# Kernel optimization log

Hardware: AMD Instinct MI355X
Metric: run time of the kernel (lower is better)

## Reference

```python
import jax, jax.numpy as jnp
import numpy as np
from itertools import product

EPS = 1e-6
P = 3  # heatmap_size; corr channels = P**3 = 27


def l2_on_axis(x, axis=1):
    return jnp.sqrt(jnp.sum(x * x, axis=axis, keepdims=True) + EPS)


def reduce_masked_mean(x, mask):
    return jnp.sum(x * mask) / (jnp.sum(mask) + EPS)


def smoothl1(d):
    a = jnp.abs(d)
    return jnp.where(a < 1.0, 0.5 * d * d, a - 0.5)


def corr3d(f0, f1):
    # 3D correlation volume, patch P^3, zero padding. (B,C,D,H,W)->(B,P^3,D,H,W)
    B, C, D, H, W = f0.shape
    pad = P // 2
    f1p = jnp.pad(f1, ((0, 0), (0, 0), (pad, pad), (pad, pad), (pad, pad)))
    outs = []
    for dz in range(P):
        for dy in range(P):
            for dx in range(P):
                s = f1p[:, :, dz:dz + D, dy:dy + H, dx:dx + W]
                outs.append(jnp.einsum('bcdhw,bcdhw->bdhw', f0, s))
    return jnp.stack(outs, axis=1)


def flow_head(cc, W1, b1, W2, b2):
    cc = jax.nn.relu(cc)
    cc = cc / (jnp.sqrt(jnp.sum(cc * cc, axis=1, keepdims=True)) + EPS)  # l2_normalize dim=1
    h = jnp.einsum('oc,bcdhw->bodhw', W1, cc) + b1[None, :, None, None, None]
    h = jnp.where(h > 0, h, 0.01 * h)  # LeakyReLU
    return jnp.einsum('oc,bcdhw->bodhw', W2, h) + b2[None, :, None, None, None]


def backwarp(feat, flow):
    # trilinear backwarp, zero padding outside; flow ch: (dx->W, dy->H, dz->D)
    B, C, D, H, W = feat.shape
    zz, yy, xx = jnp.meshgrid(jnp.arange(D, dtype=flow.dtype),
                              jnp.arange(H, dtype=flow.dtype),
                              jnp.arange(W, dtype=flow.dtype), indexing='ij')
    xs = xx[None] + flow[:, 0]
    ys = yy[None] + flow[:, 1]
    zs = zz[None] + flow[:, 2]
    x0, y0, z0 = jnp.floor(xs), jnp.floor(ys), jnp.floor(zs)
    featf = feat.reshape(B, C, D * H * W)
    out = jnp.zeros_like(feat)
    for cz, cy, cx in product((0, 1), (0, 1), (0, 1)):
        zi, yi, xi = z0 + cz, y0 + cy, x0 + cx
        w = (1 - jnp.abs(zs - zi)) * (1 - jnp.abs(ys - yi)) * (1 - jnp.abs(xs - xi))
        valid = ((zi >= 0) & (zi < D) & (yi >= 0) & (yi < H) & (xi >= 0) & (xi < W)).astype(feat.dtype)
        idx = ((jnp.clip(zi, 0, D - 1) * H + jnp.clip(yi, 0, H - 1)) * W
               + jnp.clip(xi, 0, W - 1)).astype(jnp.int32).reshape(B, -1)
        g = jnp.take_along_axis(featf, idx[:, None, :], axis=2).reshape(B, C, D, H, W)
        out = out + g * (w * valid)[:, None]
    return out


def gradient3d_abs(x):
    dz = jnp.abs(jnp.pad(x[:, :, 1:] - x[:, :, :-1], ((0, 0), (0, 0), (0, 1), (0, 0), (0, 0))))
    dy = jnp.abs(jnp.pad(x[:, :, :, 1:] - x[:, :, :, :-1], ((0, 0), (0, 0), (0, 0), (0, 1), (0, 0))))
    dx = jnp.abs(jnp.pad(x[:, :, :, :, 1:] - x[:, :, :, :, :-1], ((0, 0), (0, 0), (0, 0), (0, 0), (0, 1))))
    return dx, dy, dz


def setup_inputs() -> dict:
    key = jax.random.key(0)
    ks = jax.random.split(key, 8)
    B, C, D, H, W = 2, 32, 64, 64, 64
    return {
        'feat0': jax.random.normal(ks[0], (B, C, D, H, W), jnp.float32),
        'feat1': jax.random.normal(ks[1], (B, C, D, H, W), jnp.float32),
        'flow_g': jax.random.normal(ks[2], (B, 3, D, H, W), jnp.float32),
        'mask_g': jax.random.uniform(ks[3], (B, 1, D, H, W), jnp.float32),
        'W1': jax.random.normal(ks[4], (64, P ** 3), jnp.float32) * 0.05,
        'b1': jnp.zeros((64,), jnp.float32),
        'W2': jax.random.normal(ks[5], (3, 64), jnp.float32) * 0.05,
        'b2': jnp.zeros((3,), jnp.float32),
        'is_synth': 0,
    }


def reference(feat0, feat1, flow_g, mask_g, W1, b1, W2, b2, is_synth):
    B, C, D, H, W = feat0.shape
    # hinge loss (feat1_aligned == feat1 at iteration 0)
    hinge_vox = jax.nn.relu(0.2 - l2_on_axis(feat1 - feat0))
    hinge_mask = (jnp.sum(jnp.abs(flow_g), axis=1, keepdims=True) > 1.0).astype(feat0.dtype)
    hinge_loss = reduce_masked_mean(hinge_vox, hinge_mask)

    # single scale sc=1.0
    flow_forw = flow_head(corr3d(feat0, feat1), W1, b1, W2, b2)
    flow_back = flow_head(corr3d(feat1, feat0), W1, b1, W2, b2)

    feat1_aligned = backwarp(feat1, flow_forw)
    ones1 = jnp.ones((B, 1, D, H, W), feat0.dtype)
    valid1 = backwarp(ones1, flow_forw)
    valid0 = backwarp(ones1, flow_forw)  # faithful: source also uses flow_total_forw

    feat_diff = reduce_masked_mean(l2_on_axis(feat1_aligned - feat0), valid1 * valid0)
    warp_loss_cumu = feat_diff  # * sc (=1)

    l1_diff = jnp.mean(smoothl1(flow_forw - flow_g), axis=1, keepdims=True)
    l2_diff = jnp.mean((flow_forw - flow_g) ** 2, axis=1, keepdims=True)
    nonzero = (jnp.sum(jnp.abs(flow_g), axis=1, keepdims=True) > 0.01).astype(feat0.dtype) * mask_g
    yeszero = (1.0 - nonzero) * mask_g
    l1_bal = 0.5 * (reduce_masked_mean(l1_diff, nonzero) + reduce_masked_mean(l1_diff, yeszero))
    l2_bal = 0.5 * (reduce_masked_mean(l2_diff, nonzero) + reduce_masked_mean(l2_diff, yeszero))

    fb_al = backwarp(flow_back, jax.lax.stop_gradient(flow_forw))
    ff_al = backwarp(flow_forw, jax.lax.stop_gradient(flow_back))
    cycle_loss = jnp.mean(smoothl1(flow_forw + fb_al)) + jnp.mean(smoothl1(flow_back + ff_al))

    dx, dy, dz = gradient3d_abs(flow_forw)
    smooth_forw = jnp.mean(dx + dy + dx, axis=1, keepdims=True)  # faithful: dx counted twice
    dx, dy, dz = gradient3d_abs(flow_back)
    smooth_back = jnp.mean(dx + dy + dx, axis=1, keepdims=True)
    smooth_loss = jnp.mean((smooth_forw + smooth_back) * 0.5)

    # all hyp coefficients = 1.0; is_synth selects identical coeffs here
    total_loss = hinge_loss + cycle_loss + l1_bal + l2_bal + warp_loss_cumu + smooth_loss
    return total_loss, flow_forw
```

## Files before the change

### kernel.cpp

```cpp
#include <hip/hip_runtime.h>
#include <math.h>

#define EPSF 1e-6f

typedef __attribute__((ext_vector_type(8))) short short8;
typedef __attribute__((ext_vector_type(4))) float f32x4;

constexpr int Bn = 2, Cn = 32, Dn = 64, Hn = 64, Wn = 64;
constexpr int HW  = Hn * Wn;
constexpr int DHW = Dn * HW;
constexpr int NVOX = Bn * DHW;
constexpr size_t BS = (size_t)Cn * DHW;


__device__ inline float sl1(float d) {
    float a = fabsf(d);
    return a < 1.f ? 0.5f * d * d : a - 0.5f;
}

__device__ inline int xcd_swz(int bid, int chunk) {
    return (bid & 7) * chunk + (bid >> 3);
}

__device__ inline float dpp_left(float v) {
    int r = __builtin_amdgcn_update_dpp(0, __float_as_int(v), 0x138, 0xF, 0xF, true);
    return __int_as_float(r);
}
__device__ inline float dpp_right(float v) {
    int r = __builtin_amdgcn_update_dpp(0, __float_as_int(v), 0x130, 0xF, 0xF, true);
    return __int_as_float(r);
}

__device__ inline unsigned int bf16b(float f) {
    return (__float_as_uint(f) + 0x8000u) >> 16;
}
__device__ inline unsigned int bfpack(float lo, float hi) {
    return bf16b(lo) | ((__float_as_uint(hi) + 0x8000u) & 0xffff0000u);
}
__device__ inline float bf2f(unsigned short u) {
    return __uint_as_float((unsigned int)u << 16);
}
__device__ inline float unpk(uint2 q, int j) {
    unsigned w = (j < 2) ? q.x : q.y;
    return (j & 1) ? __uint_as_float(w & 0xffff0000u)
                   : __uint_as_float(w << 16);
}

struct PairGather {
    int   pidx[4];
    int   sel[4];
    float w0[4], w1[4];
};

__device__ inline void warp_pair_setup(float flx, float fly, float flz,
                                       int x, int y, int z,
                                       PairGather& pg, float& wsum) {
    float xs = (float)x + flx, ys = (float)y + fly, zs = (float)z + flz;
    float xf = floorf(xs), yf = floorf(ys), zf = floorf(zs);
    float fx = xs - xf, fy = ys - yf, fz = zs - zf;
    int xi = (int)xf, yi = (int)yf, zi = (int)zf;

    int x0c = min(max(xi, 0), Wn - 1);
    bool xv0 = (xi >= 0) && (xi < Wn);
    bool xv1 = (xi + 1 >= 0) && (xi + 1 < Wn);
    int sel = (xi >= 0 && xi < Wn - 1) ? 1 : 0;
    float wx0 = xv0 ? (1.f - fx) : 0.f;
    float wx1 = xv1 ? fx : 0.f;

    wsum = 0.f;
#pragma unroll
    for (int cz = 0; cz < 2; cz++) {
        int zz = zi + cz;
        bool zv = (zz >= 0) && (zz < Dn);
        int zc = min(max(zz, 0), Dn - 1);
        float wz = (cz ? fz : 1.f - fz) * (zv ? 1.f : 0.f);
#pragma unroll
        for (int cy = 0; cy < 2; cy++) {
            int yy = yi + cy;
            bool yv = (yy >= 0) && (yy < Hn);
            int yc = min(max(yy, 0), Hn - 1);
            float wy = (cy ? fy : 1.f - fy) * (yv ? 1.f : 0.f);
            int k = cz * 2 + cy;
            int sp = (zc * Hn + yc) * Wn + x0c;
            pg.pidx[k] = min(sp, DHW - 2);
            pg.sel[k] = sel;
            float wzy = wz * wy;
            pg.w0[k] = wzy * wx0;
            pg.w1[k] = wzy * wx1;
            wsum += pg.w0[k] + pg.w1[k];
        }
    }
}

__device__ inline float gather8(const float* __restrict__ slab, const PairGather& pg) {
    float g = 0.f;
#pragma unroll
    for (int k = 0; k < 4; k++) {
        float2 v = *reinterpret_cast<const float2*>(slab + pg.pidx[k]);
        float second = pg.sel[k] ? v.y : v.x;
        g = fmaf(v.x, pg.w0[k], g);
        g = fmaf(second, pg.w1[k], g);
    }
    return g;
}

__global__ void prep_kernel(const float* __restrict__ W1, ushort* __restrict__ W1bf) {
    int i = blockIdx.x * 256 + threadIdx.x;
    if (i < 64 * 32) {
        int n = i >> 5, k = i & 31;
        float val = (k < 27) ? W1[n * 27 + k] : 0.f;
        W1bf[n * 40 + k] = (ushort)bf16b(val);
    }
}

__global__ __launch_bounds__(256)
void pack_kernel(const float* __restrict__ f1, uint2* __restrict__ pk1) {
    int v = blockIdx.x * 256 + threadIdx.x;
    int b = v >> 18;
    int sp = v & (DHW - 1);
    const float* src = f1 + (size_t)b * BS + sp;
#pragma unroll
    for (int p = 0; p < 8; p++) {
        float c0 = src[(size_t)(4 * p + 0) * DHW];
        float c1 = src[(size_t)(4 * p + 1) * DHW];
        float c2 = src[(size_t)(4 * p + 2) * DHW];
        float c3 = src[(size_t)(4 * p + 3) * DHW];
        pk1[(size_t)p * NVOX + v] = make_uint2(bfpack(c0, c1), bfpack(c2, c3));
    }
}

__device__ __forceinline__ void flow_head_mfma(
        float* acc, ushort (*ccS)[64][40], int wid, int lane,
        const ushort* __restrict__ W1bf, const float* __restrict__ b1,
        const float* __restrict__ W2, const float* __restrict__ b2,
        float* __restrict__ flow_out, size_t fb0,
        float& mfx, float& mfy, float& mfz) {
    float ss = 0.f;
#pragma unroll
    for (int i = 0; i < 27; i++) {
        float r = acc[i] > 0.f ? acc[i] : 0.f;
        acc[i] = r;
        ss = fmaf(r, r, ss);
    }
    float inv = 1.0f / (sqrtf(ss) + EPSF);
#pragma unroll
    for (int i = 0; i < 27; i++) acc[i] *= inv;

    {
        unsigned int pk[16];
#pragma unroll
        for (int i = 0; i < 13; i++) pk[i] = bfpack(acc[2 * i], acc[2 * i + 1]);
        pk[13] = bfpack(acc[26], 0.f);
        pk[14] = 0u; pk[15] = 0u;
        uint2* rowp = reinterpret_cast<uint2*>(&ccS[wid][lane][0]);
#pragma unroll
        for (int i = 0; i < 8; i++) rowp[i] = make_uint2(pk[2 * i], pk[2 * i + 1]);
    }

    int c0 = lane & 15, oct = lane >> 4;

    short8 bfr[4];
#pragma unroll
    for (int t = 0; t < 4; t++)
        bfr[t] = *reinterpret_cast<const short8*>(W1bf + (size_t)(t * 16 + c0) * 40 + oct * 8);

    f32x4 b1v[4], w2f0[4], w2f1[4], w2f2[4];
#pragma unroll
    for (int mt = 0; mt < 4; mt++) {
        b1v[mt]  = *reinterpret_cast<const f32x4*>(b1 + mt * 16 + oct * 4);
        w2f0[mt] = *reinterpret_cast<const f32x4*>(W2 + mt * 16 + oct * 4);
        w2f1[mt] = *reinterpret_cast<const f32x4*>(W2 + 64 + mt * 16 + oct * 4);
        w2f2[mt] = *reinterpret_cast<const f32x4*>(W2 + 128 + mt * 16 + oct * 4);
    }
    float bb0 = b2[0], bb1 = b2[1], bb2 = b2[2];

#pragma unroll
    for (int nt = 0; nt < 4; nt++) {
        short8 afr = *reinterpret_cast<const short8*>(&ccS[wid][nt * 16 + c0][oct * 8]);
        f32x4 ac[4];
#pragma unroll
        for (int mt = 0; mt < 4; mt++) {
            f32x4 zero = {0.f, 0.f, 0.f, 0.f};
            ac[mt] = __builtin_amdgcn_mfma_f32_16x16x32_bf16(bfr[mt], afr, zero, 0, 0, 0);
        }
        float p0 = 0.f, p1 = 0.f, p2 = 0.f;
#pragma unroll
        for (int mt = 0; mt < 4; mt++) {
#pragma unroll
            for (int rg = 0; rg < 4; rg++) {
                float h = ac[mt][rg] + b1v[mt][rg];
                h = fmaxf(h, 0.01f * h);
                p0 = fmaf(w2f0[mt][rg], h, p0);
                p1 = fmaf(w2f1[mt][rg], h, p1);
                p2 = fmaf(w2f2[mt][rg], h, p2);
            }
        }
        p0 += __shfl_xor(p0, 16); p0 += __shfl_xor(p0, 32);
        p1 += __shfl_xor(p1, 16); p1 += __shfl_xor(p1, 32);
        p2 += __shfl_xor(p2, 16); p2 += __shfl_xor(p2, 32);
        if (oct == nt) {
            int vox = nt * 16 + c0;
            mfx = p0 + bb0; mfy = p1 + bb1; mfz = p2 + bb2;
            flow_out[fb0 + vox]           = mfx;
            flow_out[fb0 + DHW + vox]     = mfy;
            flow_out[fb0 + 2 * DHW + vox] = mfz;
        }
    }
}

__device__ __forceinline__ void fwd_losses_common(
        float mfx, float mfy, float mfz, float diff2,
        const float* __restrict__ flow_g, const float* __restrict__ mask_g,
        int lane, int y, int z, int b, size_t fb0, float* pv) {
    size_t fbase = fb0 + lane;
    float gx = flow_g[fbase], gy = flow_g[fbase + DHW], gz = flow_g[fbase + 2 * DHW];
    float mg = mask_g[(size_t)b * DHW + (size_t)z * HW + y * Wn + lane];

    float ag = fabsf(gx) + fabsf(gy) + fabsf(gz);
    float hmask = ag > 1.0f ? 1.f : 0.f;
    float hv = 0.2f - sqrtf(diff2 + EPSF);
    hv = hv > 0.f ? hv : 0.f;

    float dx0 = mfx - gx, dy0 = mfy - gy, dz0 = mfz - gz;
    float l1 = (sl1(dx0) + sl1(dy0) + sl1(dz0)) * (1.f / 3.f);
    float l2 = (dx0 * dx0 + dy0 * dy0 + dz0 * dz0) * (1.f / 3.f);
    float nz = (ag > 0.01f ? 1.f : 0.f) * mg;
    float yz = (1.f - nz) * mg;

    pv[0] = hv * hmask; pv[1] = hmask;
    pv[4] = l1 * nz;    pv[5] = l1 * yz;
    pv[6] = l2 * nz;    pv[7] = l2 * yz;
    pv[8] = nz;         pv[9] = yz;
}

__global__ __launch_bounds__(256)
void corr_fwd_packed(const float* __restrict__ feat0, const uint2* __restrict__ pk1,
                     const ushort* __restrict__ W1bf, const float* __restrict__ b1,
                     const float* __restrict__ W2, const float* __restrict__ b2,
                     float* __restrict__ flow_forw,
                     const float* __restrict__ flow_g, const float* __restrict__ mask_g,
                     float* __restrict__ accum, ushort* __restrict__ craw) {
    __shared__ ushort ccS[4][64][40];

    int tid = threadIdx.x;
    int lane = tid & 63;
    int wid = __builtin_amdgcn_readfirstlane(tid >> 6);

    int R = xcd_swz(blockIdx.x, 256) * 4 + wid;
    int y = R & 63, z = (R >> 6) & 63, b = R >> 12;

    const uint2* rp[9];
    float rmask[9];
    {
        int idx = 0;
#pragma unroll
        for (int dz = -1; dz <= 1; dz++) {
#pragma unroll
            for (int dy = -1; dy <= 1; dy++, idx++) {
                int zz = z + dz, yy = y + dy;
                bool valid = (zz >= 0) && (zz < Dn) && (yy >= 0) && (yy < Hn);
                int zc = min(max(zz, 0), Dn - 1);
                int yc = min(max(yy, 0), Hn - 1);
                rp[idx] = pk1 + (size_t)b * DHW + (size_t)zc * HW + (size_t)yc * Wn;
                rmask[idx] = valid ? 1.f : 0.f;
            }
        }
    }
    const float* ap = feat0 + (size_t)b * BS + (size_t)z * HW + (size_t)y * Wn;

    float C[9], TL[9], TR[9];
#pragma unroll
    for (int r = 0; r < 9; r++) { C[r] = 0.f; TL[r] = 0.f; TR[r] = 0.f; }
    float diff2 = 0.f;

#pragma unroll 1
    for (int p = 0; p < 8; p++) {
        uint2 q[9];
#pragma unroll
        for (int r = 0; r < 9; r++) q[r] = rp[r][lane];
        float a4[4];
#pragma unroll
        for (int j = 0; j < 4; j++) a4[j] = ap[(size_t)j * DHW + lane];
        ap += (size_t)4 * DHW;
#pragma unroll
        for (int r = 0; r < 9; r++) rp[r] += NVOX;

#pragma unroll
        for (int j = 0; j < 4; j++) {
            float a = a4[j];
            float aL = dpp_left(a), aR = dpp_right(a);
            float ctr = unpk(q[4], j);
            float d = ctr - a;
            diff2 = fmaf(d, d, diff2);
#pragma unroll
            for (int r = 0; r < 9; r++) {
                float rv = unpk(q[r], j);
                C[r]  = fmaf(a,  rv, C[r]);
                TL[r] = fmaf(aL, rv, TL[r]);
                TR[r] = fmaf(aR, rv, TR[r]);
            }
        }
    }

    float acc[27];
#pragma unroll
    for (int r = 0; r < 9; r++) {
        acc[r * 3 + 0] = dpp_left(TR[r]) * rmask[r];
        acc[r * 3 + 1] = C[r] * rmask[r];
        acc[r * 3 + 2] = dpp_right(TL[r]) * rmask[r];
    }

    size_t vidx = (size_t)R * 64 + lane;
#pragma unroll
    for (int i = 0; i < 27; i++)
        craw[(size_t)i * NVOX + vidx] = (ushort)bf16b(acc[i]);

    size_t fb0 = (size_t)b * 3 * DHW + (size_t)z * HW + (size_t)y * Wn;
    float mfx, mfy, mfz;
    flow_head_mfma(acc, ccS, wid, lane, W1bf, b1, W2, b2, flow_forw, fb0,
                   mfx, mfy, mfz);

    float pv[10];
    fwd_losses_common(mfx, mfy, mfz, diff2, flow_g, mask_g, lane, y, z, b, fb0, pv);

    {
        PairGather pgF; float wsum;
        warp_pair_setup(mfx, mfy, mfz, lane, y, z, pgF, wsum);
        const uint2* slab0 = pk1 + (size_t)b * DHW;
        const float* f0c = feat0 + (size_t)b * BS + (size_t)z * HW + (size_t)y * Wn + lane;
        float s = 0.f;
#pragma unroll 1
        for (int p = 0; p < 8; p++) {
            const uint2* slab = slab0 + (size_t)p * NVOX;
            float g4[4] = {0.f, 0.f, 0.f, 0.f};
#pragma unroll
            for (int k = 0; k < 4; k++) {
                uint2 q0 = slab[pgF.pidx[k]];
                uint2 q1 = slab[pgF.pidx[k] + 1];
#pragma unroll
                for (int j = 0; j < 4; j++) {
                    float v0 = unpk(q0, j);
                    float v1 = pgF.sel[k] ? unpk(q1, j) : v0;
                    g4[j] = fmaf(v0, pgF.w0[k], g4[j]);
                    g4[j] = fmaf(v1, pgF.w1[k], g4[j]);
                }
            }
#pragma unroll
            for (int j = 0; j < 4; j++) {
                float d = g4[j] - f0c[(size_t)(4 * p + j) * DHW];
                s = fmaf(d, d, s);
            }
        }
        float vm = wsum * wsum;
        pv[2] = sqrtf(s + EPSF) * vm;
        pv[3] = vm;
    }

#pragma unroll
    for (int i = 0; i < 10; i++) {
        float val = pv[i];
        for (int off = 32; off; off >>= 1) val += __shfl_down(val, off, 64);
        pv[i] = val;
    }
    __shared__ float sred[10][4];
    if (lane == 0) {
#pragma unroll
        for (int i = 0; i < 10; i++) sred[i][wid] = pv[i];
    }
    __syncthreads();
    if (tid < 10) {
        atomicAdd(&accum[tid], sred[tid][0] + sred[tid][1] + sred[tid][2] + sred[tid][3]);
    }
}

__global__ __launch_bounds__(256)
void corr_fwd_f32(const float* __restrict__ feat0, const float* __restrict__ feat1,
                  const ushort* __restrict__ W1bf, const float* __restrict__ b1,
                  const float* __restrict__ W2, const float* __restrict__ b2,
                  float* __restrict__ flow_forw,
                  const float* __restrict__ flow_g, const float* __restrict__ mask_g,
                  float* __restrict__ accum, ushort* __restrict__ craw) {
    __shared__ ushort ccS[4][64][40];

    int tid = threadIdx.x;
    int lane = tid & 63;
    int wid = __builtin_amdgcn_readfirstlane(tid >> 6);

    int R = xcd_swz(blockIdx.x, 256) * 4 + wid;
    int y = R & 63, z = (R >> 6) & 63, b = R >> 12;

    const float* rp[9];
    float rmask[9];
    {
        int idx = 0;
#pragma unroll
        for (int dz = -1; dz <= 1; dz++) {
#pragma unroll
            for (int dy = -1; dy <= 1; dy++, idx++) {
                int zz = z + dz, yy = y + dy;
                bool valid = (zz >= 0) && (zz < Dn) && (yy >= 0) && (yy < Hn);
                int zc = min(max(zz, 0), Dn - 1);
                int yc = min(max(yy, 0), Hn - 1);
                rp[idx] = feat1 + (size_t)b * BS + (size_t)zc * HW + (size_t)yc * Wn;
                rmask[idx] = valid ? 1.f : 0.f;
            }
        }
    }
    const float* ap = feat0 + (size_t)b * BS + (size_t)z * HW + (size_t)y * Wn;

    float C[9], TL[9], TR[9];
#pragma unroll
    for (int r = 0; r < 9; r++) { C[r] = 0.f; TL[r] = 0.f; TR[r] = 0.f; }
    float diff2 = 0.f;

#pragma unroll 2
    for (int c = 0; c < Cn; c++) {
        float a = ap[lane];
        float rowv[9];
#pragma unroll
        for (int r = 0; r < 9; r++) rowv[r] = rp[r][lane];
        ap += DHW;
#pragma unroll
        for (int r = 0; r < 9; r++) rp[r] += DHW;

        float aL = dpp_left(a), aR = dpp_right(a);
        float d = rowv[4] - a;
        diff2 = fmaf(d, d, diff2);
#pragma unroll
        for (int r = 0; r < 9; r++) {
            float rv = rowv[r];
            C[r]  = fmaf(a,  rv, C[r]);
            TL[r] = fmaf(aL, rv, TL[r]);
            TR[r] = fmaf(aR, rv, TR[r]);
        }
    }

    float acc[27];
#pragma unroll
    for (int r = 0; r < 9; r++) {
        acc[r * 3 + 0] = dpp_left(TR[r]) * rmask[r];
        acc[r * 3 + 1] = C[r] * rmask[r];
        acc[r * 3 + 2] = dpp_right(TL[r]) * rmask[r];
    }

    size_t vidx = (size_t)R * 64 + lane;
#pragma unroll
    for (int i = 0; i < 27; i++)
        craw[(size_t)i * NVOX + vidx] = (ushort)bf16b(acc[i]);

    size_t fb0 = (size_t)b * 3 * DHW + (size_t)z * HW + (size_t)y * Wn;
    float mfx, mfy, mfz;
    flow_head_mfma(acc, ccS, wid, lane, W1bf, b1, W2, b2, flow_forw, fb0,
                   mfx, mfy, mfz);

    float pv[10];
    fwd_losses_common(mfx, mfy, mfz, diff2, flow_g, mask_g, lane, y, z, b, fb0, pv);

    {
        PairGather pgF; float wsum;
        warp_pair_setup(mfx, mfy, mfz, lane, y, z, pgF, wsum);
        const float* f1b = feat1 + (size_t)b * BS;
        const float* f0c = feat0 + (size_t)b * BS + (size_t)z * HW + (size_t)y * Wn + lane;
        float s = 0.f;
#pragma unroll 4
        for (int c = 0; c < Cn; c++) {
            float g = gather8(f1b + (size_t)c * DHW, pgF);
            float d = g - f0c[(size_t)c * DHW];
            s = fmaf(d, d, s);
        }
        float vm = wsum * wsum;
        pv[2] = sqrtf(s + EPSF) * vm;
        pv[3] = vm;
    }

#pragma unroll
    for (int i = 0; i < 10; i++) {
        float val = pv[i];
        for (int off = 32; off; off >>= 1) val += __shfl_down(val, off, 64);
        pv[i] = val;
    }
    __shared__ float sred[10][4];
    if (lane == 0) {
#pragma unroll
        for (int i = 0; i < 10; i++) sred[i][wid] = pv[i];
    }
    __syncthreads();
    if (tid < 10) {
        atomicAdd(&accum[tid], sred[tid][0] + sred[tid][1] + sred[tid][2] + sred[tid][3]);
    }
}

__global__ __launch_bounds__(256)
void corr_bwd_kernel(const ushort* __restrict__ craw,
                     const ushort* __restrict__ W1bf, const float* __restrict__ b1,
                     const float* __restrict__ W2, const float* __restrict__ b2,
                     float* __restrict__ flow_back) {
    __shared__ ushort ccSb[4][64][40];

    int tid = threadIdx.x;
    int lane = tid & 63;
    int wid = __builtin_amdgcn_readfirstlane(tid >> 6);

    int R = xcd_swz(blockIdx.x, 256) * 4 + wid;
    int y = R & 63, z = (R >> 6) & 63, b = R >> 12;

    float acc[27];
#pragma unroll
    for (int sz = 0; sz < 3; sz++) {
#pragma unroll
        for (int sy = 0; sy < 3; sy++) {
            int zz = z + sz - 1, yy = y + sy - 1;
            bool valid = (zz >= 0) && (zz < Dn) && (yy >= 0) && (yy < Hn);
            int zc = min(max(zz, 0), Dn - 1);
            int yc = min(max(yy, 0), Hn - 1);
            float m = valid ? 1.f : 0.f;
            const ushort* rowb = craw + (size_t)b * DHW + (size_t)zc * HW + (size_t)yc * Wn + lane;
            int base = (sz * 3 + sy) * 3;
            float v0 = bf2f(rowb[(size_t)(26 - base) * NVOX]);
            float v1 = bf2f(rowb[(size_t)(25 - base) * NVOX]);
            float v2 = bf2f(rowb[(size_t)(24 - base) * NVOX]);
            acc[base + 0] = dpp_left(v0) * m;
            acc[base + 1] = v1 * m;
            acc[base + 2] = dpp_right(v2) * m;
        }
    }

    size_t fb0 = (size_t)b * 3 * DHW + (size_t)z * HW + (size_t)y * Wn;
    float mfx, mfy, mfz;
    flow_head_mfma(acc, ccSb, wid, lane, W1bf, b1, W2, b2, flow_back, fb0,
                   mfx, mfy, mfz);
}

__global__ __launch_bounds__(256)
void slim_loss_kernel(const float* __restrict__ flowf, const float* __restrict__ flowb,
                      float* __restrict__ accum) {
    int tid = threadIdx.x;
    int v = xcd_swz(blockIdx.x, 256) * 256 + tid;
    int x = v & 63, y = (v >> 6) & 63, z = (v >> 12) & 63, b = v >> 18;

    size_t sp = (size_t)z * HW + y * Wn + x;
    size_t f3 = (size_t)b * 3 * DHW + sp;

    float ffx = flowf[f3], ffy = flowf[f3 + DHW], ffz = flowf[f3 + 2 * DHW];
    float fbx = flowb[f3], fby = flowb[f3 + DHW], fbz = flowb[f3 + 2 * DHW];

    PairGather pgF; float wsumF;
    warp_pair_setup(ffx, ffy, ffz, x, y, z, pgF, wsumF);
    const float* fb_b = flowb + (size_t)b * 3 * DHW;
    float fbalx = gather8(fb_b, pgF);
    float fbaly = gather8(fb_b + DHW, pgF);
    float fbalz = gather8(fb_b + 2 * DHW, pgF);
    float cyc1 = sl1(ffx + fbalx) + sl1(ffy + fbaly) + sl1(ffz + fbalz);

    PairGather pgB; float wsumB;
    warp_pair_setup(fbx, fby, fbz, x, y, z, pgB, wsumB);
    const float* ff_b = flowf + (size_t)b * 3 * DHW;
    float ffalx = gather8(ff_b, pgB);
    float ffaly = gather8(ff_b + DHW, pgB);
    float ffalz = gather8(ff_b + 2 * DHW, pgB);
    float cyc2 = sl1(fbx + ffalx) + sl1(fby + ffaly) + sl1(fbz + ffalz);

    float sf = 0.f, sb2v = 0.f;
#pragma unroll
    for (int j = 0; j < 3; j++) {
        const float* pf = flowf + f3 + (size_t)j * DHW;
        float c0 = pf[0];
        float ddx = (x < Wn - 1) ? fabsf(pf[1] - c0) : 0.f;
        float ddy = (y < Hn - 1) ? fabsf(pf[Wn] - c0) : 0.f;
        sf += 2.f * ddx + ddy;
        const float* pb = flowb + f3 + (size_t)j * DHW;
        float c1 = pb[0];
        float ddx2 = (x < Wn - 1) ? fabsf(pb[1] - c1) : 0.f;
        float ddy2 = (y < Hn - 1) ? fabsf(pb[Wn] - c1) : 0.f;
        sb2v += 2.f * ddx2 + ddy2;
    }
    float smoothv = 0.5f * (sf * (1.f / 3.f) + sb2v * (1.f / 3.f));

    float pv[3] = { cyc1, cyc2, smoothv };
#pragma unroll
    for (int i = 0; i < 3; i++) {
        float val = pv[i];
        for (int off = 32; off; off >>= 1) val += __shfl_down(val, off, 64);
        pv[i] = val;
    }
    __shared__ float sred[3][4];
    int lane = tid & 63, wid = tid >> 6;
    if (lane == 0) {
#pragma unroll
        for (int i = 0; i < 3; i++) sred[i][wid] = pv[i];
    }
    __syncthreads();
    if (tid < 3) {
        atomicAdd(&accum[10 + tid], sred[tid][0] + sred[tid][1] + sred[tid][2] + sred[tid][3]);
    }
}

__global__ void finalize_kernel(const float* __restrict__ accum, float* __restrict__ out) {
    float hinge = accum[0] / (accum[1] + EPSF);
    float warp  = accum[2] / (accum[3] + EPSF);
    float l1b = 0.5f * (accum[4] / (accum[8] + EPSF) + accum[5] / (accum[9] + EPSF));
    float l2b = 0.5f * (accum[6] / (accum[8] + EPSF) + accum[7] / (accum[9] + EPSF));
    float n3 = 3.0f * (float)NVOX;
    float cyc = accum[10] / n3 + accum[11] / n3;
    float sm  = accum[12] / (float)NVOX;
    out[0] = hinge + cyc + l1b + l2b + warp + sm;
}

extern "C" void kernel_launch(void* const* d_in, const int* in_sizes, int n_in,
                              void* d_out, int out_size, void* d_ws, size_t ws_size,
                              hipStream_t stream) {
    const float* feat0  = (const float*)d_in[0];
    const float* feat1  = (const float*)d_in[1];
    const float* flow_g = (const float*)d_in[2];
    const float* mask_g = (const float*)d_in[3];
    const float* W1     = (const float*)d_in[4];
    const float* b1     = (const float*)d_in[5];
    const float* W2     = (const float*)d_in[6];
    const float* b2     = (const float*)d_in[7];

    float* out = (float*)d_out;
    float* accum = (float*)d_ws;
    ushort* W1bf = (ushort*)((char*)d_ws + 128);
    const size_t FLOWB_OFF = 8192;
    const size_t FLOWB_BYTES = (size_t)Bn * 3 * DHW * sizeof(float);
    float* flow_back = (float*)((char*)d_ws + FLOWB_OFF);
    const size_t CRAW_OFF = FLOWB_OFF + FLOWB_BYTES;
    const size_t CRAW_BYTES = (size_t)27 * NVOX * sizeof(ushort);
    ushort* craw = (ushort*)((char*)d_ws + CRAW_OFF);
    const size_t PK1_OFF = CRAW_OFF + CRAW_BYTES;
    const size_t PK1_BYTES = (size_t)Cn * NVOX * sizeof(ushort);
    uint2* pk1 = (uint2*)((char*)d_ws + PK1_OFF);
    float* flow_forw = out + 1;

    hipMemsetAsync(d_ws, 0, 64, stream);

    prep_kernel<<<dim3(8), dim3(256), 0, stream>>>(W1, W1bf);

    if (ws_size >= PK1_OFF + PK1_BYTES) {
        pack_kernel<<<dim3(NVOX / 256), dim3(256), 0, stream>>>(feat1, pk1);
        corr_fwd_packed<<<dim3(NVOX / 256), dim3(256), 0, stream>>>(
            feat0, pk1, W1bf, b1, W2, b2, flow_forw, flow_g, mask_g, accum, craw);
    } else {
        corr_fwd_f32<<<dim3(NVOX / 256), dim3(256), 0, stream>>>(
            feat0, feat1, W1bf, b1, W2, b2, flow_forw, flow_g, mask_g, accum, craw);
    }
    corr_bwd_kernel<<<dim3(NVOX / 256), dim3(256), 0, stream>>>(
        craw, W1bf, b1, W2, b2, flow_back);
    slim_loss_kernel<<<dim3(NVOX / 256), dim3(256), 0, stream>>>(flow_forw, flow_back, accum);
    finalize_kernel<<<1, 1, 0, stream>>>(accum, out);
}
```

Measured before the change: 139.9 us.

## Pack correlation cache in triplets, merge neighbor gathers, fuse backward cycle loss

The correlation cache is now stored as 9 planes of packed uint2 (three bf16 values per voxel) instead of 27 separate ushort planes. This turns 27 scattered 2-byte stores and 9×3 loads into 9 wide accesses each. The forward warp gather fetches two adjacent packed voxels with one 16-byte load instead of two 8-byte loads. The backward cycle-consistency term is computed inside the backward kernel from the flow it has just produced, so the slim loss kernel no longer reloads flow_back or runs that second gather. The packed layout spends a padding slot per group, giving slightly more bytes per voxel, and the 16-byte load relies on 8-byte alignment.

```diff
diff --git a/kernel.cpp b/kernel.cpp
--- a/kernel.cpp
+++ b/kernel.cpp
@@ -5,6 +5,7 @@
 
 typedef __attribute__((ext_vector_type(8))) short short8;
 typedef __attribute__((ext_vector_type(4))) float f32x4;
+typedef __attribute__((ext_vector_type(4), aligned(8))) unsigned int uint4a;
 
 constexpr int Bn = 2, Cn = 32, Dn = 64, Hn = 64, Wn = 64;
 constexpr int HW  = Hn * Wn;
@@ -40,10 +41,15 @@
 __device__ inline float bf2f(unsigned short u) {
     return __uint_as_float((unsigned int)u << 16);
 }
+__device__ inline float lo16(unsigned w) { return __uint_as_float(w << 16); }
+__device__ inline float hi16(unsigned w) { return __uint_as_float(w & 0xffff0000u); }
 __device__ inline float unpk(uint2 q, int j) {
     unsigned w = (j < 2) ? q.x : q.y;
-    return (j & 1) ? __uint_as_float(w & 0xffff0000u)
-                   : __uint_as_float(w << 16);
+    return (j & 1) ? hi16(w) : lo16(w);
+}
+__device__ inline float unpk4(uint4a q, int half, int j) {
+    unsigned w = (j < 2) ? q[2 * half] : q[2 * half + 1];
+    return (j & 1) ? hi16(w) : lo16(w);
 }
 
 struct PairGather {
@@ -233,13 +239,21 @@
     pv[8] = nz;         pv[9] = yz;
 }
 
+__device__ __forceinline__ void craw_store(uint2* __restrict__ cg, size_t vidx,
+                                           const float* acc) {
+#pragma unroll
+    for (int g = 0; g < 9; g++)
+        cg[(size_t)g * NVOX + vidx] =
+            make_uint2(bfpack(acc[3 * g], acc[3 * g + 1]), bfpack(acc[3 * g + 2], 0.f));
+}
+
 __global__ __launch_bounds__(256)
 void corr_fwd_packed(const float* __restrict__ feat0, const uint2* __restrict__ pk1,
                      const ushort* __restrict__ W1bf, const float* __restrict__ b1,
                      const float* __restrict__ W2, const float* __restrict__ b2,
                      float* __restrict__ flow_forw,
                      const float* __restrict__ flow_g, const float* __restrict__ mask_g,
-                     float* __restrict__ accum, ushort* __restrict__ craw) {
+                     float* __restrict__ accum, uint2* __restrict__ cg) {
     __shared__ ushort ccS[4][64][40];
 
     int tid = threadIdx.x;
@@ -310,10 +324,7 @@
         acc[r * 3 + 2] = dpp_right(TL[r]) * rmask[r];
     }
 
-    size_t vidx = (size_t)R * 64 + lane;
-#pragma unroll
-    for (int i = 0; i < 27; i++)
-        craw[(size_t)i * NVOX + vidx] = (ushort)bf16b(acc[i]);
+    craw_store(cg, (size_t)R * 64 + lane, acc);
 
     size_t fb0 = (size_t)b * 3 * DHW + (size_t)z * HW + (size_t)y * Wn;
     float mfx, mfy, mfz;
@@ -335,12 +346,11 @@
             float g4[4] = {0.f, 0.f, 0.f, 0.f};
 #pragma unroll
             for (int k = 0; k < 4; k++) {
-                uint2 q0 = slab[pgF.pidx[k]];
-                uint2 q1 = slab[pgF.pidx[k] + 1];
+                uint4a q = *reinterpret_cast<const uint4a*>(slab + pgF.pidx[k]);
 #pragma unroll
                 for (int j = 0; j < 4; j++) {
-                    float v0 = unpk(q0, j);
-                    float v1 = pgF.sel[k] ? unpk(q1, j) : v0;
+                    float v0 = unpk4(q, 0, j);
+                    float v1 = pgF.sel[k] ? unpk4(q, 1, j) : v0;
                     g4[j] = fmaf(v0, pgF.w0[k], g4[j]);
                     g4[j] = fmaf(v1, pgF.w1[k], g4[j]);
                 }
@@ -379,7 +389,7 @@
                   const float* __restrict__ W2, const float* __restrict__ b2,
                   float* __restrict__ flow_forw,
                   const float* __restrict__ flow_g, const float* __restrict__ mask_g,
-                  float* __restrict__ accum, ushort* __restrict__ craw) {
+                  float* __restrict__ accum, uint2* __restrict__ cg) {
     __shared__ ushort ccS[4][64][40];
 
     int tid = threadIdx.x;
@@ -443,10 +453,7 @@
         acc[r * 3 + 2] = dpp_right(TL[r]) * rmask[r];
     }
 
-    size_t vidx = (size_t)R * 64 + lane;
-#pragma unroll
-    for (int i = 0; i < 27; i++)
-        craw[(size_t)i * NVOX + vidx] = (ushort)bf16b(acc[i]);
+    craw_store(cg, (size_t)R * 64 + lane, acc);
 
     size_t fb0 = (size_t)b * 3 * DHW + (size_t)z * HW + (size_t)y * Wn;
     float mfx, mfy, mfz;
@@ -491,10 +498,11 @@
 }
 
 __global__ __launch_bounds__(256)
-void corr_bwd_kernel(const ushort* __restrict__ craw,
+void corr_bwd_kernel(const uint2* __restrict__ cg,
                      const ushort* __restrict__ W1bf, const float* __restrict__ b1,
                      const float* __restrict__ W2, const float* __restrict__ b2,
-                     float* __restrict__ flow_back) {
+                     float* __restrict__ flow_back, const float* __restrict__ flow_forw,
+                     float* __restrict__ accum) {
     __shared__ ushort ccSb[4][64][40];
 
     int tid = threadIdx.x;
@@ -509,19 +517,22 @@
     for (int sz = 0; sz < 3; sz++) {
 #pragma unroll
         for (int sy = 0; sy < 3; sy++) {
+            int cell = sz * 3 + sy;
             int zz = z + sz - 1, yy = y + sy - 1;
             bool valid = (zz >= 0) && (zz < Dn) && (yy >= 0) && (yy < Hn);
             int zc = min(max(zz, 0), Dn - 1);
             int yc = min(max(yy, 0), Hn - 1);
             float m = valid ? 1.f : 0.f;
-            const ushort* rowb = craw + (size_t)b * DHW + (size_t)zc * HW + (size_t)yc * Wn + lane;
-            int base = (sz * 3 + sy) * 3;
-            float v0 = bf2f(rowb[(size_t)(26 - base) * NVOX]);
-            float v1 = bf2f(rowb[(size_t)(25 - base) * NVOX]);
-            float v2 = bf2f(rowb[(size_t)(24 - base) * NVOX]);
-            acc[base + 0] = dpp_left(v0) * m;
-            acc[base + 1] = v1 * m;
-            acc[base + 2] = dpp_right(v2) * m;
+            int gb = 8 - cell;
+            uint2 q = cg[(size_t)gb * NVOX + (size_t)b * DHW +
+                         (size_t)zc * HW + (size_t)yc * Wn + lane];
+            float s0 = lo16(q.x);
+            float s1 = hi16(q.x);
+            float s2 = lo16(q.y);
+            int base = cell * 3;
+            acc[base + 0] = dpp_left(s2) * m;
+            acc[base + 1] = s1 * m;
+            acc[base + 2] = dpp_right(s0) * m;
         }
     }
 
@@ -529,6 +540,21 @@
     float mfx, mfy, mfz;
     flow_head_mfma(acc, ccSb, wid, lane, W1bf, b1, W2, b2, flow_back, fb0,
                    mfx, mfy, mfz);
+
+    PairGather pgB; float wsumB;
+    warp_pair_setup(mfx, mfy, mfz, lane, y, z, pgB, wsumB);
+    const float* ff_b = flow_forw + (size_t)b * 3 * DHW;
+    float ffalx = gather8(ff_b, pgB);
+    float ffaly = gather8(ff_b + DHW, pgB);
+    float ffalz = gather8(ff_b + 2 * DHW, pgB);
+    float cyc2 = sl1(mfx + ffalx) + sl1(mfy + ffaly) + sl1(mfz + ffalz);
+
+    for (int off = 32; off; off >>= 1) cyc2 += __shfl_down(cyc2, off, 64);
+    __shared__ float s2red[4];
+    if (lane == 0) s2red[wid] = cyc2;
+    __syncthreads();
+    if (tid == 0)
+        atomicAdd(&accum[11], s2red[0] + s2red[1] + s2red[2] + s2red[3]);
 }
 
 __global__ __launch_bounds__(256)
@@ -542,7 +568,6 @@
     size_t f3 = (size_t)b * 3 * DHW + sp;
 
     float ffx = flowf[f3], ffy = flowf[f3 + DHW], ffz = flowf[f3 + 2 * DHW];
-    float fbx = flowb[f3], fby = flowb[f3 + DHW], fbz = flowb[f3 + 2 * DHW];
 
     PairGather pgF; float wsumF;
     warp_pair_setup(ffx, ffy, ffz, x, y, z, pgF, wsumF);
@@ -551,14 +576,6 @@
     float fbaly = gather8(fb_b + DHW, pgF);
     float fbalz = gather8(fb_b + 2 * DHW, pgF);
     float cyc1 = sl1(ffx + fbalx) + sl1(ffy + fbaly) + sl1(ffz + fbalz);
-
-    PairGather pgB; float wsumB;
-    warp_pair_setup(fbx, fby, fbz, x, y, z, pgB, wsumB);
-    const float* ff_b = flowf + (size_t)b * 3 * DHW;
-    float ffalx = gather8(ff_b, pgB);
-    float ffaly = gather8(ff_b + DHW, pgB);
-    float ffalz = gather8(ff_b + 2 * DHW, pgB);
-    float cyc2 = sl1(fbx + ffalx) + sl1(fby + ffaly) + sl1(fbz + ffalz);
 
     float sf = 0.f, sb2v = 0.f;
 #pragma unroll
@@ -576,22 +593,23 @@
     }
     float smoothv = 0.5f * (sf * (1.f / 3.f) + sb2v * (1.f / 3.f));
 
-    float pv[3] = { cyc1, cyc2, smoothv };
-#pragma unroll
-    for (int i = 0; i < 3; i++) {
+    float pv[2] = { cyc1, smoothv };
+#pragma unroll
+    for (int i = 0; i < 2; i++) {
         float val = pv[i];
         for (int off = 32; off; off >>= 1) val += __shfl_down(val, off, 64);
         pv[i] = val;
     }
-    __shared__ float sred[3][4];
+    __shared__ float sred[2][4];
     int lane = tid & 63, wid = tid >> 6;
     if (lane == 0) {
 #pragma unroll
-        for (int i = 0; i < 3; i++) sred[i][wid] = pv[i];
+        for (int i = 0; i < 2; i++) sred[i][wid] = pv[i];
     }
     __syncthreads();
-    if (tid < 3) {
-        atomicAdd(&accum[10 + tid], sred[tid][0] + sred[tid][1] + sred[tid][2] + sred[tid][3]);
+    if (tid < 2) {
+        int dst = (tid == 0) ? 10 : 12;
+        atomicAdd(&accum[dst], sred[tid][0] + sred[tid][1] + sred[tid][2] + sred[tid][3]);
     }
 }
 
@@ -625,8 +643,8 @@
     const size_t FLOWB_BYTES = (size_t)Bn * 3 * DHW * sizeof(float);
     float* flow_back = (float*)((char*)d_ws + FLOWB_OFF);
     const size_t CRAW_OFF = FLOWB_OFF + FLOWB_BYTES;
-    const size_t CRAW_BYTES = (size_t)27 * NVOX * sizeof(ushort);
-    ushort* craw = (ushort*)((char*)d_ws + CRAW_OFF);
+    const size_t CRAW_BYTES = (size_t)9 * NVOX * sizeof(uint2);
+    uint2* cg = (uint2*)((char*)d_ws + CRAW_OFF);
     const size_t PK1_OFF = CRAW_OFF + CRAW_BYTES;
     const size_t PK1_BYTES = (size_t)Cn * NVOX * sizeof(ushort);
     uint2* pk1 = (uint2*)((char*)d_ws + PK1_OFF);
@@ -639,13 +657,13 @@
     if (ws_size >= PK1_OFF + PK1_BYTES) {
         pack_kernel<<<dim3(NVOX / 256), dim3(256), 0, stream>>>(feat1, pk1);
         corr_fwd_packed<<<dim3(NVOX / 256), dim3(256), 0, stream>>>(
-            feat0, pk1, W1bf, b1, W2, b2, flow_forw, flow_g, mask_g, accum, craw);
+            feat0, pk1, W1bf, b1, W2, b2, flow_forw, flow_g, mask_g, accum, cg);
     } else {
         corr_fwd_f32<<<dim3(NVOX / 256), dim3(256), 0, stream>>>(
-            feat0, feat1, W1bf, b1, W2, b2, flow_forw, flow_g, mask_g, accum, craw);
+            feat0, feat1, W1bf, b1, W2, b2, flow_forw, flow_g, mask_g, accum, cg);
     }
     corr_bwd_kernel<<<dim3(NVOX / 256), dim3(256), 0, stream>>>(
-        craw, W1bf, b1, W2, b2, flow_back);
+        cg, W1bf, b1, W2, b2, flow_back, flow_forw, accum);
     slim_loss_kernel<<<dim3(NVOX / 256), dim3(256), 0, stream>>>(flow_forw, flow_back, accum);
     finalize_kernel<<<1, 1, 0, stream>>>(accum, out);
 }
```

After: 158.6 us. +13.4%, slower.
